# Performance work log

Hardware: AMD Instinct MI355X
Metric: run time of the kernel (lower is better)

The kernel has to match this reference:

```python
import jax, jax.numpy as jnp
import numpy as np

EPS = 1e-5

def _conv1x1(x, w, b):
    # x: (b,c,h,w), w: (o,c) -> (b,o,h,w)
    return jnp.einsum('bchw,oc->bohw', x, w) + b[None, :, None, None]

def _maxpool2(x):
    b, c, h, w = x.shape
    return x.reshape(b, c, h // 2, 2, w // 2, 2).max(axis=(3, 5))

def setup_inputs() -> dict:
    key = jax.random.key(0)
    ks = jax.random.split(key, 11)
    C, CI, H, W, B = 256, 128, 64, 64, 8
    s = 0.05
    return {
        'x': jax.random.normal(ks[0], (B, C, H, W), jnp.float32),
        'Wg': jax.random.normal(ks[1], (CI, C), jnp.float32) * s,
        'bg': jax.random.normal(ks[2], (CI,), jnp.float32) * s,
        'Wt': jax.random.normal(ks[3], (CI, C), jnp.float32) * s,
        'bt': jax.random.normal(ks[4], (CI,), jnp.float32) * s,
        'Wp': jax.random.normal(ks[5], (CI, C), jnp.float32) * s,
        'bp': jax.random.normal(ks[6], (CI,), jnp.float32) * s,
        'Ww': jax.random.normal(ks[7], (C, CI), jnp.float32) * s,
        'bw': jax.random.normal(ks[8], (C,), jnp.float32) * s,
        'gamma': jax.random.normal(ks[9], (C,), jnp.float32),
        'beta': jax.random.normal(ks[10], (C,), jnp.float32),
    }

def reference(x, Wg, bg, Wt, bt, Wp, bp, Ww, bw, gamma, beta):
    b, C, H, W = x.shape
    CI = Wg.shape[0]
    # g and phi are sub-sampled by 2x2 max pool -> M = (H/2)*(W/2); theta keeps N = H*W
    g_x = _maxpool2(_conv1x1(x, Wg, bg)).reshape(b, CI, -1).transpose(0, 2, 1)   # (b,M,ci)
    theta_x = _conv1x1(x, Wt, bt).reshape(b, CI, -1).transpose(0, 2, 1)          # (b,N,ci)
    phi_x = _maxpool2(_conv1x1(x, Wp, bp)).reshape(b, CI, -1)                    # (b,ci,M)
    f = jnp.einsum('bnc,bcm->bnm', theta_x, phi_x)                               # (b,N,M)
    f_div_C = jax.nn.softmax(f, axis=-1)
    y = jnp.einsum('bnm,bmc->bnc', f_div_C, g_x)                                 # (b,N,ci)
    y = y.transpose(0, 2, 1).reshape(b, CI, H, W)
    # W: 1x1 conv + BatchNorm2d (training mode: batch statistics, biased var)
    wy = _conv1x1(y, Ww, bw)
    mean = wy.mean(axis=(0, 2, 3), keepdims=True)
    var = ((wy - mean) ** 2).mean(axis=(0, 2, 3), keepdims=True)
    wy = (wy - mean) * jax.lax.rsqrt(var + EPS)
    wy = wy * gamma[None, :, None, None] + beta[None, :, None, None]
    z = wy + x
    # self.avg_pool is AdaptiveMaxPool2d(1): global spatial max
    return z.max(axis=(2, 3), keepdims=True)
```

## Files before the change

### kernel.cpp

```cpp
#include <hip/hip_runtime.h>
#include <hip/hip_bf16.h>
#include <stdint.h>

using f32x4  = __attribute__((ext_vector_type(4))) float;
using bf16x8 = __attribute__((ext_vector_type(8))) short;
using short4v = __attribute__((ext_vector_type(4))) short;

#define DEVINL static __device__ __forceinline__

DEVINL short f2bf(float f) {
    union { float f; uint32_t u; } v; v.f = f;
    uint32_t r = (v.u + 0x7FFFu + ((v.u >> 16) & 1u)) >> 16;
    return (short)(uint16_t)r;
}
DEVINL float bf2f(short s) {
    union { uint32_t u; float f; } v; v.u = ((uint32_t)(uint16_t)s) << 16;
    return v.f;
}
DEVINL float fexp2(float x) {
    float r;
    asm("v_exp_f32 %0, %1" : "=v"(r) : "v"(x));
    return r;
}

DEVINL void gld16(const short* g, short* l) {
    __builtin_amdgcn_global_load_lds(
        (const __attribute__((address_space(1))) unsigned int*)g,
        (__attribute__((address_space(3))) unsigned int*)l, 16, 0, 0);
}

#define LOG2E 1.44269504f

__global__ __launch_bounds__(256) void k0_prep(
        const float* __restrict__ Wg, const float* __restrict__ Wt, const float* __restrict__ Wp,
        const float* __restrict__ bg, const float* __restrict__ bt, const float* __restrict__ bp,
        const float* __restrict__ Ww,
        short* __restrict__ W_all, short* __restrict__ Ww16, float* __restrict__ b_all) {
    int i = blockIdx.x * 256 + threadIdx.x;
    if (i < 384 * 256) {
        int r = i >> 8, c = i & 255;
        float v = (r < 128) ? Wg[r * 256 + c]
                : (r < 256) ? Wt[(r - 128) * 256 + c] * LOG2E
                            : Wp[(r - 256) * 256 + c];
        W_all[i] = f2bf(v);
    } else if (i < 384 * 256 + 256 * 128) {
        int j = i - 384 * 256;
        Ww16[j] = f2bf(Ww[j]);
    }
    if (i < 384) {
        b_all[i] = (i < 128) ? bg[i] : (i < 256) ? bt[i - 128] * LOG2E : bp[i - 256];
    }
}

__global__ __launch_bounds__(256) void k1_conv(const float* __restrict__ x,
        const short* __restrict__ W_all, const float* __restrict__ b_all,
        short* __restrict__ OutT, short* __restrict__ Kmat, short* __restrict__ Vmat) {
    __shared__ short xs[128 * 32];
    __shared__ short obuf[128 * 128];
    const int ntile = blockIdx.x;
    const int otile = blockIdx.y;
    const int b     = blockIdx.z;
    const int tid  = threadIdx.x;
    const int lane = tid & 63;
    const int wave = tid >> 6;
    const int wn = wave >> 1, wo = wave & 1;
    const int l15 = lane & 15, lh = lane >> 4;

    f32x4 acc[4][4];
    #pragma unroll
    for (int i = 0; i < 4; i++)
        #pragma unroll
        for (int j = 0; j < 4; j++) acc[i][j] = f32x4{0.f, 0.f, 0.f, 0.f};

    const int n0 = ntile * 128;
    const int ob = otile * 128 + wo * 64;
    const float* xb = x + (size_t)b * 256 * 4096;

    const int srow_base = (lane & 15) + wave * 16;
    const int sc0 = (lane >> 4) * 8;

    for (int kt = 0; kt < 8; kt++) {
        __syncthreads();
        #pragma unroll
        for (int p = 0; p < 2; p++) {
            int row = srow_base + p * 64;
            const float* xp = xb + (size_t)(kt * 32 + sc0) * 4096 + n0 + row;
            bf16x8 w8;
            #pragma unroll
            for (int j = 0; j < 8; j++) w8[j] = f2bf(xp[(size_t)j * 4096]);
            int ch = (sc0 >> 3) ^ ((row >> 1) & 3);
            *(bf16x8*)&xs[row * 32 + ch * 8] = w8;
        }
        __syncthreads();

        bf16x8 a[4], w[4];
        #pragma unroll
        for (int nf = 0; nf < 4; nf++) {
            int row = wn * 64 + nf * 16 + l15;
            int ch  = lh ^ ((row >> 1) & 3);
            a[nf] = *(const bf16x8*)&xs[row * 32 + ch * 8];
        }
        #pragma unroll
        for (int of = 0; of < 4; of++)
            w[of] = *(const bf16x8*)(W_all + (size_t)(ob + of * 16 + l15) * 256 + kt * 32 + lh * 8);
        #pragma unroll
        for (int nf = 0; nf < 4; nf++)
            #pragma unroll
            for (int of = 0; of < 4; of++)
                acc[nf][of] = __builtin_amdgcn_mfma_f32_16x16x32_bf16(a[nf], w[of], acc[nf][of], 0, 0, 0);
    }

    #pragma unroll
    for (int of = 0; of < 4; of++) {
        int ocol = wo * 64 + of * 16 + l15;
        float bias = b_all[otile * 128 + ocol];
        #pragma unroll
        for (int nf = 0; nf < 4; nf++)
            #pragma unroll
            for (int r = 0; r < 4; r++) {
                int n  = wn * 64 + nf * 16 + lh * 4 + r;
                int ch = (ocol >> 3) ^ (n & 15);
                obuf[n * 128 + ch * 8 + (ocol & 7)] = f2bf(acc[nf][of][r] + bias);
            }
    }
    __syncthreads();

    if (otile == 1) {
        #pragma unroll
        for (int p = 0; p < 8; p++) {
            int n  = wave * 4 + lh + p * 16;
            int ch = l15 ^ (n & 15);
            bf16x8 v = *(const bf16x8*)&obuf[n * 128 + ch * 8];
            *(bf16x8*)(OutT + ((size_t)b * 4096 + n0 + n) * 128 + l15 * 8) = v;
        }
    } else if (otile == 2) {
        const int wp = tid >> 3;
        const int cc = (tid & 7) * 16;
        short* kdst = Kmat + ((size_t)b * 1024 + ntile * 32 + wp) * 128 + cc;
        #pragma unroll
        for (int cblk = 0; cblk < 2; cblk++) {
            const int chunk = (cc >> 3) + cblk;
            float mx[8];
            #pragma unroll
            for (int j = 0; j < 8; j++) mx[j] = -1e30f;
            #pragma unroll
            for (int q4 = 0; q4 < 4; q4++) {
                int n = (q4 >> 1) * 64 + 2 * wp + (q4 & 1);
                bf16x8 v = *(const bf16x8*)&obuf[n * 128 + ((chunk ^ (n & 15)) * 8)];
                #pragma unroll
                for (int j = 0; j < 8; j++) mx[j] = fmaxf(mx[j], bf2f(v[j]));
            }
            bf16x8 vo;
            #pragma unroll
            for (int j = 0; j < 8; j++) vo[j] = f2bf(mx[j]);
            *(bf16x8*)(kdst + cblk * 8) = vo;
        }
    } else {
        const int c   = tid >> 1;
        const int wp0 = (tid & 1) * 16;
        const int chb = c >> 3, cl = c & 7;
        #pragma unroll
        for (int half = 0; half < 2; half++) {
            bf16x8 vo;
            #pragma unroll
            for (int j = 0; j < 8; j++) {
                int wp = wp0 + half * 8 + j;
                float mx = -1e30f;
                #pragma unroll
                for (int q4 = 0; q4 < 4; q4++) {
                    int n = (q4 >> 1) * 64 + 2 * wp + (q4 & 1);
                    mx = fmaxf(mx, bf2f(obuf[n * 128 + ((chb ^ (n & 15)) * 8) + cl]));
                }
                vo[j] = f2bf(mx);
            }
            *(bf16x8*)(Vmat + ((size_t)b * 128 + c) * 1024 + ntile * 32 + wp0 + half * 8) = vo;
        }
    }
}

__global__ __launch_bounds__(256) void k3_attn(const short* __restrict__ OutT,
        const short* __restrict__ Kmat, const short* __restrict__ Vmat,
        const short* __restrict__ Ww16, const float* __restrict__ bw,
        short* __restrict__ wy) {
    __shared__ short sK[2][64 * 128];
    __shared__ short sV[2][128 * 64];
    __shared__ short sP[4][16 * 64];

    const int bid = blockIdx.x;
    const int b   = bid & 7;
    const int nt  = bid >> 3;
    const int tid = threadIdx.x;
    const int lane = tid & 63;
    const int wave = tid >> 6;
    const int l15 = lane & 15, lh = lane >> 4;
    const int n0 = nt * 64 + wave * 16;

    const short* Kb = Kmat + (size_t)b * 1024 * 128;
    const short* Vb = Vmat + (size_t)b * 128 * 1024;
    short* sPw = sP[wave];

    auto STAGE = [&](int t, int bufi) {
        const int m0 = t * 64;
        #pragma unroll
        for (int i = 0; i < 4; i++) {
            const int segb = (i * 4 + wave) * 64;
            const int rowK = (segb >> 4) + (lane >> 4);
            const int chkK = lane & 15;
            gld16(Kb + (size_t)(m0 + rowK) * 128 + ((chkK ^ (rowK & 15)) << 3),
                  &sK[bufi][segb * 8]);
            const int rowV = (segb >> 3) + (lane >> 3);
            const int chkV = lane & 7;
            gld16(Vb + (size_t)rowV * 1024 + m0 + ((chkV ^ (rowV & 7)) << 3),
                  &sV[bufi][segb * 8]);
        }
    };

    bf16x8 q[4];
    {
        const short* qrow = OutT + ((size_t)b * 4096 + n0 + l15) * 128;
        #pragma unroll
        for (int ks = 0; ks < 4; ks++)
            q[ks] = *(const bf16x8*)(qrow + ks * 32 + lh * 8);
    }

    f32x4 y[8];
    #pragma unroll
    for (int cf = 0; cf < 8; cf++) y[cf] = f32x4{0.f, 0.f, 0.f, 0.f};
    float mrun = -1e30f, lrun = 0.f;

    STAGE(0, 0);
    int cur = 0;

    for (int t = 0; t < 16; t++) {
        if (t < 15) {
            STAGE(t + 1, cur ^ 1);
            asm volatile("s_waitcnt vmcnt(8)" ::: "memory");
        } else {
            asm volatile("s_waitcnt vmcnt(0)" ::: "memory");
        }
        __builtin_amdgcn_s_barrier();
        __builtin_amdgcn_sched_barrier(0);

        const short* cK = sK[cur];
        const short* cV = sV[cur];

        f32x4 S[4];
        #pragma unroll
        for (int mf = 0; mf < 4; mf++) S[mf] = f32x4{0.f, 0.f, 0.f, 0.f};
        #pragma unroll
        for (int ks = 0; ks < 4; ks++) {
            bf16x8 kf[4];
            #pragma unroll
            for (int mf = 0; mf < 4; mf++) {
                int mrow = mf * 16 + l15;
                int jj   = ks * 4 + lh;
                kf[mf] = *(const bf16x8*)&cK[mrow * 128 + ((jj ^ (mrow & 15)) << 3)];
            }
            __builtin_amdgcn_s_setprio(1);
            #pragma unroll
            for (int mf = 0; mf < 4; mf++)
                S[mf] = __builtin_amdgcn_mfma_f32_16x16x32_bf16(kf[mf], q[ks], S[mf], 0, 0, 0);
            __builtin_amdgcn_s_setprio(0);
        }

        float pm = S[0][0];
        #pragma unroll
        for (int mf = 0; mf < 4; mf++)
            #pragma unroll
            for (int r = 0; r < 4; r++) pm = fmaxf(pm, S[mf][r]);
        pm = fmaxf(pm, __shfl_xor(pm, 16));
        pm = fmaxf(pm, __shfl_xor(pm, 32));

        if (__any(pm > mrun + 8.656f)) {
            float mnew  = fmaxf(mrun, pm);
            float alpha = fexp2(mrun - mnew);
            mrun = mnew;
            lrun *= alpha;
            float aR[4];
            #pragma unroll
            for (int r = 0; r < 4; r++) aR[r] = __shfl(alpha, lh * 4 + r);
            #pragma unroll
            for (int cf = 0; cf < 8; cf++)
                #pragma unroll
                for (int r = 0; r < 4; r++) y[cf][r] *= aR[r];
        }
        float rs = 0.f;
        #pragma unroll
        for (int mf = 0; mf < 4; mf++)
            #pragma unroll
            for (int r = 0; r < 4; r++) {
                float p = fexp2(S[mf][r] - mrun);
                S[mf][r] = p;
                rs += p;
            }
        rs += __shfl_xor(rs, 16);
        rs += __shfl_xor(rs, 32);
        lrun += rs;

        #pragma unroll
        for (int mf = 0; mf < 4; mf++) {
            short4v pk = { f2bf(S[mf][0]), f2bf(S[mf][1]), f2bf(S[mf][2]), f2bf(S[mf][3]) };
            *(short4v*)&sPw[(l15 << 6) + (((mf * 4 + lh) ^ l15) << 2)] = pk;
        }

        #pragma unroll
        for (int ks2 = 0; ks2 < 2; ks2++) {
            int u0 = ks2 * 8 + lh * 2;
            short4v lo = *(const short4v*)&sPw[(l15 << 6) + (((u0)     ^ l15) << 2)];
            short4v hi = *(const short4v*)&sPw[(l15 << 6) + (((u0 + 1) ^ l15) << 2)];
            bf16x8 pa = { lo.x, lo.y, lo.z, lo.w, hi.x, hi.y, hi.z, hi.w };
            int jj = ks2 * 4 + lh;
            __builtin_amdgcn_s_setprio(1);
            #pragma unroll
            for (int cf = 0; cf < 8; cf++) {
                int crow = cf * 16 + l15;
                bf16x8 vf = *(const bf16x8*)&cV[crow * 64 + ((jj ^ (crow & 7)) << 3)];
                y[cf] = __builtin_amdgcn_mfma_f32_16x16x32_bf16(pa, vf, y[cf], 0, 0, 0);
            }
            __builtin_amdgcn_s_setprio(0);
        }

        __builtin_amdgcn_sched_barrier(0);
        __builtin_amdgcn_s_barrier();
        cur ^= 1;
    }

    float linv[4];
    #pragma unroll
    for (int r = 0; r < 4; r++) linv[r] = 1.f / __shfl(lrun, lh * 4 + r);

    bf16x8 by[4];
    #pragma unroll
    for (int h = 0; h < 2; h++) {
        #pragma unroll
        for (int cfl = 0; cfl < 4; cfl++) {
            int cf = h * 4 + cfl;
            #pragma unroll
            for (int r = 0; r < 4; r++) {
                int n = lh * 4 + r;
                int chunk4 = cfl * 4 + (l15 >> 2);
                sPw[n * 64 + ((chunk4 ^ n) << 2) + (l15 & 3)] = f2bf(y[cf][r] * linv[r]);
            }
        }
        #pragma unroll
        for (int ks2 = 0; ks2 < 2; ks2++) {
            int u0 = ks2 * 8 + lh * 2;
            short4v lo = *(const short4v*)&sPw[(l15 << 6) + (((u0)     ^ l15) << 2)];
            short4v hi = *(const short4v*)&sPw[(l15 << 6) + (((u0 + 1) ^ l15) << 2)];
            by[h * 2 + ks2] = bf16x8{ lo.x, lo.y, lo.z, lo.w, hi.x, hi.y, hi.z, hi.w };
        }
    }

    #pragma unroll
    for (int of = 0; of < 16; of++) {
        bf16x8 aw[4];
        #pragma unroll
        for (int ks = 0; ks < 4; ks++)
            aw[ks] = *(const bf16x8*)(Ww16 + (size_t)(of * 16 + l15) * 128 + ks * 32 + lh * 8);
        f32x4 acc = f32x4{0.f, 0.f, 0.f, 0.f};
        #pragma unroll
        for (int ks = 0; ks < 4; ks++)
            acc = __builtin_amdgcn_mfma_f32_16x16x32_bf16(aw[ks], by[ks], acc, 0, 0, 0);
        #pragma unroll
        for (int r = 0; r < 4; r++) {
            int o = of * 16 + lh * 4 + r;
            wy[((size_t)b * 256 + o) * 4096 + n0 + l15] = f2bf(acc[r] + bw[o]);
        }
    }
}

__global__ __launch_bounds__(256) void k4s_stats(const short* __restrict__ wy,
        float* __restrict__ stats) {
    const int o = blockIdx.x;
    const int tid = threadIdx.x;
    float s = 0.f, s2 = 0.f;
    #pragma unroll
    for (int b = 0; b < 8; b++) {
        const short* p = wy + ((size_t)b * 256 + o) * 4096;
        #pragma unroll
        for (int i = 0; i < 2; i++) {
            bf16x8 v = *(const bf16x8*)(p + (tid + i * 256) * 8);
            #pragma unroll
            for (int j = 0; j < 8; j++) {
                float f = bf2f(v[j]);
                s += f; s2 += f * f;
            }
        }
    }
    #pragma unroll
    for (int off = 1; off < 64; off <<= 1) { s += __shfl_xor(s, off); s2 += __shfl_xor(s2, off); }
    __shared__ float red[4][2];
    if ((tid & 63) == 0) { red[tid >> 6][0] = s; red[tid >> 6][1] = s2; }
    __syncthreads();
    if (tid == 0) {
        stats[o * 2]     = red[0][0] + red[1][0] + red[2][0] + red[3][0];
        stats[o * 2 + 1] = red[0][1] + red[1][1] + red[2][1] + red[3][1];
    }
}

__global__ __launch_bounds__(256) void k5_bnmax(const short* __restrict__ wy,
        const float* __restrict__ x, const float* __restrict__ stats,
        const float* __restrict__ gamma, const float* __restrict__ beta,
        float* __restrict__ outp) {
    int b = blockIdx.x >> 8;
    int o = blockIdx.x & 255;
    int tid = threadIdx.x;
    float mean = stats[o * 2] * (1.f / 32768.f);
    float var  = stats[o * 2 + 1] * (1.f / 32768.f) - mean * mean;
    float rstd = rsqrtf(var + 1e-5f);
    float A = rstd * gamma[o];
    float B = beta[o] - mean * A;
    const short* pw = wy + ((size_t)b * 256 + o) * 4096;
    const float* px = x + ((size_t)b * 256 + o) * 4096;
    float mx = -1e30f;
    #pragma unroll
    for (int j = 0; j < 2; j++) {
        int e = (tid + j * 256) * 8;
        bf16x8 w8 = *(const bf16x8*)(pw + e);
        float4 xa = *(const float4*)(px + e);
        float4 xb = *(const float4*)(px + e + 4);
        mx = fmaxf(mx, bf2f(w8[0]) * A + B + xa.x);
        mx = fmaxf(mx, bf2f(w8[1]) * A + B + xa.y);
        mx = fmaxf(mx, bf2f(w8[2]) * A + B + xa.z);
        mx = fmaxf(mx, bf2f(w8[3]) * A + B + xa.w);
        mx = fmaxf(mx, bf2f(w8[4]) * A + B + xb.x);
        mx = fmaxf(mx, bf2f(w8[5]) * A + B + xb.y);
        mx = fmaxf(mx, bf2f(w8[6]) * A + B + xb.z);
        mx = fmaxf(mx, bf2f(w8[7]) * A + B + xb.w);
    }
    #pragma unroll
    for (int off = 1; off < 64; off <<= 1) mx = fmaxf(mx, __shfl_xor(mx, off));
    __shared__ float red[4];
    if ((tid & 63) == 0) red[tid >> 6] = mx;
    __syncthreads();
    if (tid == 0)
        outp[b * 256 + o] = fmaxf(fmaxf(red[0], red[1]), fmaxf(red[2], red[3]));
}

extern "C" void kernel_launch(void* const* d_in, const int* in_sizes, int n_in,
                              void* d_out, int out_size, void* d_ws, size_t ws_size,
                              hipStream_t stream) {
    const float* x     = (const float*)d_in[0];
    const float* Wg    = (const float*)d_in[1];
    const float* bg    = (const float*)d_in[2];
    const float* Wt    = (const float*)d_in[3];
    const float* bt    = (const float*)d_in[4];
    const float* Wp    = (const float*)d_in[5];
    const float* bp    = (const float*)d_in[6];
    const float* Ww    = (const float*)d_in[7];
    const float* bw    = (const float*)d_in[8];
    const float* gamma = (const float*)d_in[9];
    const float* beta  = (const float*)d_in[10];
    float* outp = (float*)d_out;

    char* ws = (char*)d_ws;
    size_t off = 0;
    auto alloc = [&](size_t bytes) -> void* {
        void* p = ws + off;
        off = (off + bytes + 255) & ~(size_t)255;
        return p;
    };
    short* W_all = (short*)alloc((size_t)384 * 256 * 2);
    short* Ww16  = (short*)alloc((size_t)256 * 128 * 2);
    float* b_all = (float*)alloc((size_t)384 * 4);
    short* OutT  = (short*)alloc((size_t)8 * 4096 * 128 * 2);
    short* Kmat  = (short*)alloc((size_t)8 * 1024 * 128 * 2);
    short* Vmat  = (short*)alloc((size_t)8 * 128 * 1024 * 2);
    short* wy    = (short*)alloc((size_t)8 * 256 * 4096 * 2);
    float* stats = (float*)alloc((size_t)256 * 2 * 4);

    k0_prep<<<512, 256, 0, stream>>>(Wg, Wt, Wp, bg, bt, bp, Ww, W_all, Ww16, b_all);
    k1_conv<<<dim3(32, 3, 8), 256, 0, stream>>>(x, W_all, b_all, OutT, Kmat, Vmat);
    k3_attn<<<512, 256, 0, stream>>>(OutT, Kmat, Vmat, Ww16, bw, wy);
    k4s_stats<<<256, 256, 0, stream>>>(wy, stats);
    k5_bnmax<<<2048, 256, 0, stream>>>(wy, x, stats, gamma, beta, outp);
}
```

Baseline: 97.55 us.

## Restructure attention epilogue W-projection for block-wide output split and coalesced stores

The attention kernel's final 1x1 conv epilogue is reorganized. Each wave previously computed all 256 output channels for its own 16 rows and wrote scattered 2-byte stores to wy. Now the normalized y tile for the whole 64-row block is shared through LDS. Each wave computes 64 output channels across all 64 rows, so each wave loads only a quarter of Ww. Results are staged in padded LDS and written as 16-byte coalesced row segments. This adds a block-wide barrier and reuses the K/V shared buffers as scratch.

```diff
diff --git a/kernel.cpp b/kernel.cpp
--- a/kernel.cpp
+++ b/kernel.cpp
@@ -182,9 +182,10 @@
         const short* __restrict__ Kmat, const short* __restrict__ Vmat,
         const short* __restrict__ Ww16, const float* __restrict__ bw,
         short* __restrict__ wy) {
-    __shared__ short sK[2][64 * 128];
-    __shared__ short sV[2][128 * 64];
-    __shared__ short sP[4][16 * 64];
+    __shared__ short smem[36864];
+    short* const sKb = smem;
+    short* const sVb = smem + 16384;
+    short* const sPb = smem + 32768;
 
     const int bid = blockIdx.x;
     const int b   = bid & 7;
@@ -193,11 +194,12 @@
     const int lane = tid & 63;
     const int wave = tid >> 6;
     const int l15 = lane & 15, lh = lane >> 4;
-    const int n0 = nt * 64 + wave * 16;
+    const int nblk = nt * 64;
+    const int n0 = nblk + wave * 16;
 
     const short* Kb = Kmat + (size_t)b * 1024 * 128;
     const short* Vb = Vmat + (size_t)b * 128 * 1024;
-    short* sPw = sP[wave];
+    short* sPw = sPb + wave * 1024;
 
     auto STAGE = [&](int t, int bufi) {
         const int m0 = t * 64;
@@ -207,11 +209,11 @@
             const int rowK = (segb >> 4) + (lane >> 4);
             const int chkK = lane & 15;
             gld16(Kb + (size_t)(m0 + rowK) * 128 + ((chkK ^ (rowK & 15)) << 3),
-                  &sK[bufi][segb * 8]);
+                  sKb + bufi * 8192 + segb * 8);
             const int rowV = (segb >> 3) + (lane >> 3);
             const int chkV = lane & 7;
             gld16(Vb + (size_t)rowV * 1024 + m0 + ((chkV ^ (rowV & 7)) << 3),
-                  &sV[bufi][segb * 8]);
+                  sVb + bufi * 8192 + segb * 8);
         }
     };
 
@@ -241,8 +243,8 @@
         __builtin_amdgcn_s_barrier();
         __builtin_amdgcn_sched_barrier(0);
 
-        const short* cK = sK[cur];
-        const short* cV = sV[cur];
+        const short* cK = sKb + cur * 8192;
+        const short* cV = sVb + cur * 8192;
 
         f32x4 S[4];
         #pragma unroll
@@ -329,43 +331,56 @@
     #pragma unroll
     for (int r = 0; r < 4; r++) linv[r] = 1.f / __shfl(lrun, lh * 4 + r);
 
-    bf16x8 by[4];
-    #pragma unroll
-    for (int h = 0; h < 2; h++) {
-        #pragma unroll
-        for (int cfl = 0; cfl < 4; cfl++) {
-            int cf = h * 4 + cfl;
+    short* const Yt = smem;
+    #pragma unroll
+    for (int cf = 0; cf < 8; cf++) {
+        int c = cf * 16 + l15;
+        #pragma unroll
+        for (int r = 0; r < 4; r++) {
+            int n = wave * 16 + lh * 4 + r;
+            Yt[n * 128 + (((c >> 3) ^ (n & 15)) << 3) + (c & 7)] = f2bf(y[cf][r] * linv[r]);
+        }
+    }
+    __syncthreads();
+
+    bf16x8 by[4][4];
+    #pragma unroll
+    for (int nf = 0; nf < 4; nf++)
+        #pragma unroll
+        for (int ks = 0; ks < 4; ks++) {
+            int n  = nf * 16 + l15;
+            int kc = ks * 4 + lh;
+            by[nf][ks] = *(const bf16x8*)&Yt[n * 128 + ((kc ^ (n & 15)) << 3)];
+        }
+
+    short* const sOut = smem + 8192 + wave * 4608;
+    const int obase = wave * 64;
+    #pragma unroll
+    for (int of = 0; of < 4; of++) {
+        bf16x8 aw[4];
+        #pragma unroll
+        for (int ks = 0; ks < 4; ks++)
+            aw[ks] = *(const bf16x8*)(Ww16 + (size_t)(obase + of * 16 + l15) * 128 + ks * 32 + lh * 8);
+        #pragma unroll
+        for (int nf = 0; nf < 4; nf++) {
+            f32x4 acc = f32x4{0.f, 0.f, 0.f, 0.f};
+            #pragma unroll
+            for (int ks = 0; ks < 4; ks++)
+                acc = __builtin_amdgcn_mfma_f32_16x16x32_bf16(aw[ks], by[nf][ks], acc, 0, 0, 0);
             #pragma unroll
             for (int r = 0; r < 4; r++) {
-                int n = lh * 4 + r;
-                int chunk4 = cfl * 4 + (l15 >> 2);
-                sPw[n * 64 + ((chunk4 ^ n) << 2) + (l15 & 3)] = f2bf(y[cf][r] * linv[r]);
-            }
-        }
-        #pragma unroll
-        for (int ks2 = 0; ks2 < 2; ks2++) {
-            int u0 = ks2 * 8 + lh * 2;
-            short4v lo = *(const short4v*)&sPw[(l15 << 6) + (((u0)     ^ l15) << 2)];
-            short4v hi = *(const short4v*)&sPw[(l15 << 6) + (((u0 + 1) ^ l15) << 2)];
-            by[h * 2 + ks2] = bf16x8{ lo.x, lo.y, lo.z, lo.w, hi.x, hi.y, hi.z, hi.w };
-        }
-    }
-
-    #pragma unroll
-    for (int of = 0; of < 16; of++) {
-        bf16x8 aw[4];
-        #pragma unroll
-        for (int ks = 0; ks < 4; ks++)
-            aw[ks] = *(const bf16x8*)(Ww16 + (size_t)(of * 16 + l15) * 128 + ks * 32 + lh * 8);
-        f32x4 acc = f32x4{0.f, 0.f, 0.f, 0.f};
-        #pragma unroll
-        for (int ks = 0; ks < 4; ks++)
-            acc = __builtin_amdgcn_mfma_f32_16x16x32_bf16(aw[ks], by[ks], acc, 0, 0, 0);
-        #pragma unroll
-        for (int r = 0; r < 4; r++) {
-            int o = of * 16 + lh * 4 + r;
-            wy[((size_t)b * 256 + o) * 4096 + n0 + l15] = f2bf(acc[r] + bw[o]);
-        }
+                int o_loc = of * 16 + lh * 4 + r;
+                sOut[o_loc * 72 + nf * 16 + l15] = f2bf(acc[r] + bw[obase + o_loc]);
+            }
+        }
+    }
+
+    #pragma unroll
+    for (int p = 0; p < 8; p++) {
+        int o_loc = p * 8 + (lane >> 3);
+        int n8    = (lane & 7) * 8;
+        bf16x8 v = *(const bf16x8*)&sOut[o_loc * 72 + n8];
+        *(bf16x8*)(wy + ((size_t)b * 256 + obase + o_loc) * 4096 + nblk + n8) = v;
     }
 }
 
```

New measurement: 88.93 us. -8.8%, faster.
